# Kernel optimization log

Hardware: AMD Instinct MI355X
Metric: run time of the kernel (lower is better)

## Reference

```python
import jax, jax.numpy as jnp
import numpy as np

B, S, DM, H, DK, DV = 2, 2048, 1024, 16, 64, 64

def setup_inputs() -> dict:
    key = jax.random.key(0)
    ks = jax.random.split(key, 12)
    s = 0.02
    return {
        "Q": jax.random.normal(ks[0], (B, S, DM), jnp.float32),
        "K": jax.random.normal(ks[1], (B, S, DM), jnp.float32),
        "V": jax.random.normal(ks[2], (B, S, DM), jnp.float32),
        "mask": jax.random.randint(ks[3], (B, S, S), 0, 2).astype(bool),
        "wq": jax.random.normal(ks[4], (DM, H * DK), jnp.float32) * s,
        "bq": jnp.zeros((H * DK,), jnp.float32),
        "wk": jax.random.normal(ks[5], (DM, H * DK), jnp.float32) * s,
        "bk": jnp.zeros((H * DK,), jnp.float32),
        "wv": jax.random.normal(ks[6], (DM, H * DV), jnp.float32) * s,
        "bv": jnp.zeros((H * DV,), jnp.float32),
        "wo": jax.random.normal(ks[7], (H * DV, DM), jnp.float32) * s,
        "bo": jnp.zeros((DM,), jnp.float32),
    }

def reference(Q, K, V, mask, wq, bq, wk, bk, wv, bv, wo, bo):
    b = Q.shape[0]
    # projections -> [b, h, s, d]
    q = (Q @ wq + bq).reshape(b, -1, H, DK).transpose(0, 2, 1, 3)
    k = (K @ wk + bk).reshape(b, -1, H, DK).transpose(0, 2, 1, 3)
    v = (V @ wv + bv).reshape(b, -1, H, DV).transpose(0, 2, 1, 3)
    # scaled dot-product attention with boolean mask (True = masked out)
    scores = jnp.einsum("bhqd,bhkd->bhqk", q, k) / jnp.sqrt(jnp.float32(DK))
    scores = jnp.where(mask[:, None, :, :], jnp.float32(-1e9), scores)
    attn = jax.nn.softmax(scores, axis=-1)  # [b,h,s,s]
    ctx = jnp.einsum("bhqk,bhkd->bhqd", attn, v)
    ctx = ctx.transpose(0, 2, 1, 3).reshape(b, -1, H * DV)
    out = ctx @ wo + bo  # [b, s, d_model]
    return out, attn
```

## Files before the change

kernel.cpp:

```cpp
#include <hip/hip_runtime.h>

typedef unsigned short u16;
typedef unsigned int u32;
typedef unsigned long long u64;
typedef __attribute__((ext_vector_type(8))) short bf16x8;
typedef __attribute__((ext_vector_type(4))) float f32x4;

#define NB 2
#define NS 2048
#define NDM 1024
#define NH 16

#define MFMA_B16(a, b, c) __builtin_amdgcn_mfma_f32_16x16x32_bf16(a, b, c, 0, 0, 0)

__device__ __forceinline__ u16 f2bf(float f) {
  union { float f; unsigned u; } v; v.f = f;
  return (u16)((v.u + 0x7fffu + ((v.u >> 16) & 1u)) >> 16);
}

__global__ __launch_bounds__(256) void cast_bf16(const float* __restrict__ in,
                                                 u16* __restrict__ out, int n4) {
  int i = blockIdx.x * 256 + threadIdx.x;
  if (i < n4) {
    const float4 v = reinterpret_cast<const float4*>(in)[i];
    ushort4 o; o.x = f2bf(v.x); o.y = f2bf(v.y); o.z = f2bf(v.z); o.w = f2bf(v.w);
    reinterpret_cast<ushort4*>(out)[i] = o;
  }
}

__global__ __launch_bounds__(256) void transpose_w(const float* __restrict__ in,
                                                   u16* __restrict__ out) {
  __shared__ float tile[32][33];
  int bx = blockIdx.x, by = blockIdx.y;
  int x = threadIdx.x & 31, y0 = threadIdx.x >> 5;
#pragma unroll
  for (int i = 0; i < 4; i++) {
    int y = y0 + i * 8;
    tile[y][x] = in[(by * 32 + y) * NDM + bx * 32 + x];
  }
  __syncthreads();
#pragma unroll
  for (int i = 0; i < 4; i++) {
    int y = y0 + i * 8;
    out[(bx * 32 + y) * NDM + by * 32 + x] = f2bf(tile[x][y]);
  }
}

__global__ __launch_bounds__(256) void mask2bits(const u32* __restrict__ mask, u32* __restrict__ mb) {
  int idx = blockIdx.x * 256 + threadIdx.x;
  u32 mw0 = mask[threadIdx.x & 63];
  bool floatmode = (__ballot(mw0 == 0x3F800000u) != 0ull);
  bool bytemode = !floatmode && (__ballot((mw0 >> 8) != 0u) != 0ull);
  int row = idx >> 6;
  int wword = idx & 63;
  u32 bits = 0;
  if (!bytemode) {
    const uint4* p = reinterpret_cast<const uint4*>(mask + (size_t)row * 2048 + wword * 32);
#pragma unroll
    for (int i = 0; i < 8; i++) {
      uint4 v = p[i];
      bits |= (v.x ? 1u : 0u) << (i * 4 + 0);
      bits |= (v.y ? 1u : 0u) << (i * 4 + 1);
      bits |= (v.z ? 1u : 0u) << (i * 4 + 2);
      bits |= (v.w ? 1u : 0u) << (i * 4 + 3);
    }
  } else {
    const uint4* p = reinterpret_cast<const uint4*>(
        reinterpret_cast<const unsigned char*>(mask) + (size_t)row * 2048 + wword * 32);
#pragma unroll
    for (int i = 0; i < 2; i++) {
      uint4 v = p[i];
      u32 wsv[4] = {v.x, v.y, v.z, v.w};
#pragma unroll
      for (int j = 0; j < 4; j++)
#pragma unroll
        for (int kq = 0; kq < 4; kq++)
          bits |= ((((wsv[j] >> (kq * 8)) & 0xffu) != 0u) ? 1u : 0u) << (i * 16 + j * 4 + kq);
    }
  }
  mb[idx] = bits;
}

struct GArgs { const u16* X; const u16* W; const float* bias; void* out; int mode; float scale; };

__global__ __launch_bounds__(256, 2) void gemm_bt(GArgs g0, GArgs g1, GArgs g2) {
  GArgs ga = (blockIdx.z == 0) ? g0 : (blockIdx.z == 1 ? g1 : g2);
  const int K = 1024, N = 1024;
  __shared__ u16 As[128 * 32];
  __shared__ u16 Bs[128 * 32];
  const int t = threadIdx.x, w = t >> 6, l = t & 63;
  const int m0 = blockIdx.x * 128, n0 = blockIdx.y * 128;
  const int wm = (w >> 1) * 64, wn = (w & 1) * 64;
  const f32x4 fz = {0.f, 0.f, 0.f, 0.f};
  f32x4 acc[4][4];
#pragma unroll
  for (int i = 0; i < 4; i++)
#pragma unroll
    for (int j = 0; j < 4; j++) acc[i][j] = fz;

  for (int k0 = 0; k0 < K; k0 += 32) {
#pragma unroll
    for (int i = 0; i < 2; i++) {
      int idx = i * 256 + w * 64 + l;
      int r = idx >> 2, c = (idx & 3) * 8;
      __builtin_amdgcn_global_load_lds(
          reinterpret_cast<const unsigned*>(ga.X + (size_t)(m0 + r) * K + k0 + c),
          reinterpret_cast<unsigned*>(&As[(i * 256 + w * 64) * 8]), 16, 0, 0);
      __builtin_amdgcn_global_load_lds(
          reinterpret_cast<const unsigned*>(ga.W + (size_t)(n0 + r) * K + k0 + c),
          reinterpret_cast<unsigned*>(&Bs[(i * 256 + w * 64) * 8]), 16, 0, 0);
    }
    __syncthreads();
    bf16x8 af[4], bfr[4];
#pragma unroll
    for (int mt = 0; mt < 4; mt++)
      af[mt] = *reinterpret_cast<const bf16x8*>(&As[(wm + mt * 16 + (l & 15)) * 32 + (l >> 4) * 8]);
#pragma unroll
    for (int nt = 0; nt < 4; nt++)
      bfr[nt] = *reinterpret_cast<const bf16x8*>(&Bs[(wn + nt * 16 + (l & 15)) * 32 + (l >> 4) * 8]);
#pragma unroll
    for (int mt = 0; mt < 4; mt++)
#pragma unroll
      for (int nt = 0; nt < 4; nt++)
        acc[mt][nt] = MFMA_B16(af[mt], bfr[nt], acc[mt][nt]);
    __syncthreads();
  }

#pragma unroll
  for (int nt = 0; nt < 4; nt++) {
    int n = n0 + wn + nt * 16 + (l & 15);
    float bias = ga.bias[n];
#pragma unroll
    for (int mt = 0; mt < 4; mt++) {
      int mb = m0 + wm + mt * 16 + ((l >> 4) << 2);
#pragma unroll
      for (int r = 0; r < 4; r++) {
        int m = mb + r;
        float v = (acc[mt][nt][r] + bias) * ga.scale;
        if (ga.mode == 2) {
          reinterpret_cast<float*>(ga.out)[(size_t)m * N + n] = v;
        } else {
          int b = m >> 11, s = m & 2047, h = n >> 6, d = n & 63;
          if (ga.mode == 0)
            reinterpret_cast<u16*>(ga.out)[(((size_t)(b * NH + h) * NS + s) << 6) + d] = f2bf(v);
          else
            reinterpret_cast<u16*>(ga.out)[((size_t)(b * NH + h) * 64 + d) * NS + s] = f2bf(v);
        }
      }
    }
  }
}

__global__ __launch_bounds__(256, 4) void attn_kernel(
    const u16* __restrict__ qh, const u16* __restrict__ kh, const u16* __restrict__ vT,
    const u32* __restrict__ mb, float* __restrict__ attn, u16* __restrict__ ctx) {
  __shared__ u16 Ks[2][32 * 64];
  __shared__ u16 Vs[2][64 * 32];
  __shared__ u16 Ps[4][16 * 40];
  __shared__ float Pf[4][16 * 36];
  const int tid = threadIdx.x, w = tid >> 6, l = tid & 63;
  int id = blockIdx.x;
  int wgid = (id & 7) * 128 + (id >> 3);
  int qt = wgid & 31, pr = wgid >> 5;
  int h = pr & 15, b = pr >> 4;
  const size_t head = (size_t)b * NH + h;
  const u16* qp = qh + head * NS * 64;
  const u16* kp = kh + head * NS * 64;
  const u16* vp = vT + head * 64 * NS;
  const int qr0 = qt * 64 + w * 16;
  const int lo = l & 15, hi = l >> 4;
  const int rbase = hi << 2;
  const f32x4 fz = {0.f, 0.f, 0.f, 0.f};

  bf16x8 aq0, aq1;
  {
    const u16* p = qp + (size_t)(qr0 + lo) * 64 + hi * 8;
    aq0 = *reinterpret_cast<const bf16x8*>(p);
    aq1 = *reinterpret_cast<const bf16x8*>(p + 32);
  }
  const u32* mrow = mb + ((size_t)b * NS + qr0 + rbase) * 64;

  const int k_row = tid >> 3, k_slot = tid & 7;
  const u16* ksrc0 = kp + (size_t)k_row * 64 + ((k_slot ^ (k_row & 7)) * 8);
  const int v_dv = tid >> 2, v_slot = tid & 3;
  const u16* vsrc0 = vp + (size_t)v_dv * NS + ((v_slot ^ ((v_dv >> 1) & 3)) * 8);

  const int sxk = lo & 7;
  const int sxv = (lo >> 1) & 3;

  float rs0 = 0.f, rs1 = 0.f, rs2 = 0.f, rs3 = 0.f;

  __builtin_amdgcn_global_load_lds(reinterpret_cast<const unsigned*>(ksrc0),
                                   reinterpret_cast<unsigned*>(&Ks[0][w * 512]), 16, 0, 0);
  asm volatile("s_waitcnt vmcnt(0)" ::: "memory");
  __builtin_amdgcn_s_barrier();
  asm volatile("" ::: "memory");

  for (int t = 0; t < 64; ++t) {
    const u16* kbase = &Ks[t & 1][0];
    u16* kdst = &Ks[(t + 1) & 1][w * 512];
    __builtin_amdgcn_global_load_lds(
        reinterpret_cast<const unsigned*>(ksrc0 + (size_t)(t + 1) * 2048),
        reinterpret_cast<unsigned*>(kdst), 16, 0, 0);
    asm volatile("" ::: "memory");
    u32 m0 = mrow[t], m1 = mrow[64 + t], m2 = mrow[128 + t], m3 = mrow[192 + t];
    bf16x8 b00 = *reinterpret_cast<const bf16x8*>(&kbase[(lo) * 64 + ((hi ^ sxk) * 8)]);
    bf16x8 b01 = *reinterpret_cast<const bf16x8*>(&kbase[(lo) * 64 + (((4 + hi) ^ sxk) * 8)]);
    bf16x8 b10 = *reinterpret_cast<const bf16x8*>(&kbase[(16 + lo) * 64 + ((hi ^ sxk) * 8)]);
    bf16x8 b11 = *reinterpret_cast<const bf16x8*>(&kbase[(16 + lo) * 64 + (((4 + hi) ^ sxk) * 8)]);
    f32x4 s0 = MFMA_B16(aq1, b01, MFMA_B16(aq0, b00, fz));
    f32x4 s1 = MFMA_B16(aq1, b11, MFMA_B16(aq0, b10, fz));
    rs0 += ((m0 >> lo) & 1u) ? 0.f : __expf(s0[0]);
    rs1 += ((m1 >> lo) & 1u) ? 0.f : __expf(s0[1]);
    rs2 += ((m2 >> lo) & 1u) ? 0.f : __expf(s0[2]);
    rs3 += ((m3 >> lo) & 1u) ? 0.f : __expf(s0[3]);
    int bit1 = 16 + lo;
    rs0 += ((m0 >> bit1) & 1u) ? 0.f : __expf(s1[0]);
    rs1 += ((m1 >> bit1) & 1u) ? 0.f : __expf(s1[1]);
    rs2 += ((m2 >> bit1) & 1u) ? 0.f : __expf(s1[2]);
    rs3 += ((m3 >> bit1) & 1u) ? 0.f : __expf(s1[3]);
    asm volatile("s_waitcnt vmcnt(4)" ::: "memory");
    __builtin_amdgcn_s_barrier();
    asm volatile("" ::: "memory");
  }

  {
    float v;
    v = rs0; v += __shfl_xor(v, 1); v += __shfl_xor(v, 2); v += __shfl_xor(v, 4); v += __shfl_xor(v, 8);
    rs0 = 1.f / fmaxf(v, 1e-30f);
    v = rs1; v += __shfl_xor(v, 1); v += __shfl_xor(v, 2); v += __shfl_xor(v, 4); v += __shfl_xor(v, 8);
    rs1 = 1.f / fmaxf(v, 1e-30f);
    v = rs2; v += __shfl_xor(v, 1); v += __shfl_xor(v, 2); v += __shfl_xor(v, 4); v += __shfl_xor(v, 8);
    rs2 = 1.f / fmaxf(v, 1e-30f);
    v = rs3; v += __shfl_xor(v, 1); v += __shfl_xor(v, 2); v += __shfl_xor(v, 4); v += __shfl_xor(v, 8);
    rs3 = 1.f / fmaxf(v, 1e-30f);
  }

  f32x4 c0 = fz, c1 = fz, c2 = fz, c3 = fz;
  float* abase = attn + (head * NS + qr0) * NS;
  float* pfw = &Pf[w][0];
  u16* psw = &Ps[w][0];
  const int srow = l >> 2, schunk = l & 3;

  __builtin_amdgcn_global_load_lds(reinterpret_cast<const unsigned*>(ksrc0),
                                   reinterpret_cast<unsigned*>(&Ks[0][w * 512]), 16, 0, 0);
  __builtin_amdgcn_global_load_lds(reinterpret_cast<const unsigned*>(vsrc0),
                                   reinterpret_cast<unsigned*>(&Vs[0][w * 512]), 16, 0, 0);
  asm volatile("s_waitcnt vmcnt(0)" ::: "memory");
  __builtin_amdgcn_s_barrier();
  asm volatile("" ::: "memory");

  for (int t = 0; t < 64; ++t) {
    const u16* kbase = &Ks[t & 1][0];
    const u16* vbase = &Vs[t & 1][0];
    u16* kdst = &Ks[(t + 1) & 1][w * 512];
    u16* vdst = &Vs[(t + 1) & 1][w * 512];
    __builtin_amdgcn_global_load_lds(
        reinterpret_cast<const unsigned*>(ksrc0 + (size_t)(t + 1) * 2048),
        reinterpret_cast<unsigned*>(kdst), 16, 0, 0);
    __builtin_amdgcn_global_load_lds(
        reinterpret_cast<const unsigned*>(vsrc0 + (size_t)(t + 1) * 32),
        reinterpret_cast<unsigned*>(vdst), 16, 0, 0);
    asm volatile("" ::: "memory");
    u32 m0 = mrow[t], m1 = mrow[64 + t], m2 = mrow[128 + t], m3 = mrow[192 + t];
    bf16x8 b00 = *reinterpret_cast<const bf16x8*>(&kbase[(lo) * 64 + ((hi ^ sxk) * 8)]);
    bf16x8 b01 = *reinterpret_cast<const bf16x8*>(&kbase[(lo) * 64 + (((4 + hi) ^ sxk) * 8)]);
    bf16x8 b10 = *reinterpret_cast<const bf16x8*>(&kbase[(16 + lo) * 64 + ((hi ^ sxk) * 8)]);
    bf16x8 b11 = *reinterpret_cast<const bf16x8*>(&kbase[(16 + lo) * 64 + (((4 + hi) ^ sxk) * 8)]);
    f32x4 s0 = MFMA_B16(aq1, b01, MFMA_B16(aq0, b00, fz));
    f32x4 s1 = MFMA_B16(aq1, b11, MFMA_B16(aq0, b10, fz));
    float p;
    p = ((m0 >> lo) & 1u) ? 0.f : __expf(s0[0]) * rs0;
    pfw[(rbase + 0) * 36 + lo] = p; psw[(rbase + 0) * 40 + lo] = f2bf(p);
    p = ((m1 >> lo) & 1u) ? 0.f : __expf(s0[1]) * rs1;
    pfw[(rbase + 1) * 36 + lo] = p; psw[(rbase + 1) * 40 + lo] = f2bf(p);
    p = ((m2 >> lo) & 1u) ? 0.f : __expf(s0[2]) * rs2;
    pfw[(rbase + 2) * 36 + lo] = p; psw[(rbase + 2) * 40 + lo] = f2bf(p);
    p = ((m3 >> lo) & 1u) ? 0.f : __expf(s0[3]) * rs3;
    pfw[(rbase + 3) * 36 + lo] = p; psw[(rbase + 3) * 40 + lo] = f2bf(p);
    int bit1 = 16 + lo;
    p = ((m0 >> bit1) & 1u) ? 0.f : __expf(s1[0]) * rs0;
    pfw[(rbase + 0) * 36 + 16 + lo] = p; psw[(rbase + 0) * 40 + 16 + lo] = f2bf(p);
    p = ((m1 >> bit1) & 1u) ? 0.f : __expf(s1[1]) * rs1;
    pfw[(rbase + 1) * 36 + 16 + lo] = p; psw[(rbase + 1) * 40 + 16 + lo] = f2bf(p);
    p = ((m2 >> bit1) & 1u) ? 0.f : __expf(s1[2]) * rs2;
    pfw[(rbase + 2) * 36 + 16 + lo] = p; psw[(rbase + 2) * 40 + 16 + lo] = f2bf(p);
    p = ((m3 >> bit1) & 1u) ? 0.f : __expf(s1[3]) * rs3;
    pfw[(rbase + 3) * 36 + 16 + lo] = p; psw[(rbase + 3) * 40 + 16 + lo] = f2bf(p);
    bf16x8 pa = *reinterpret_cast<const bf16x8*>(&psw[lo * 40 + hi * 8]);
    bf16x8 v0 = *reinterpret_cast<const bf16x8*>(&vbase[(lo) * 32 + ((hi ^ sxv) * 8)]);
    bf16x8 v1 = *reinterpret_cast<const bf16x8*>(&vbase[(16 + lo) * 32 + ((hi ^ sxv) * 8)]);
    bf16x8 v2 = *reinterpret_cast<const bf16x8*>(&vbase[(32 + lo) * 32 + ((hi ^ sxv) * 8)]);
    bf16x8 v3 = *reinterpret_cast<const bf16x8*>(&vbase[(48 + lo) * 32 + ((hi ^ sxv) * 8)]);
    c0 = MFMA_B16(pa, v0, c0);
    c1 = MFMA_B16(pa, v1, c1);
    c2 = MFMA_B16(pa, v2, c2);
    c3 = MFMA_B16(pa, v3, c3);
    f32x4 o0 = *reinterpret_cast<const f32x4*>(&pfw[srow * 36 + schunk * 4]);
    f32x4 o1 = *reinterpret_cast<const f32x4*>(&pfw[srow * 36 + (schunk + 4) * 4]);
    *reinterpret_cast<f32x4*>(abase + (size_t)srow * NS + t * 32 + schunk * 4) = o0;
    *reinterpret_cast<f32x4*>(abase + (size_t)srow * NS + t * 32 + (schunk + 4) * 4) = o1;
    asm volatile("s_waitcnt vmcnt(6)" ::: "memory");
    __builtin_amdgcn_s_barrier();
    asm volatile("" ::: "memory");
  }

#define CTXW(cv, ct)                                                                   \
  {                                                                                    \
    ctx[((size_t)b * NS + qr0 + rbase + 0) * 1024 + h * 64 + (ct)*16 + lo] = f2bf(cv[0]); \
    ctx[((size_t)b * NS + qr0 + rbase + 1) * 1024 + h * 64 + (ct)*16 + lo] = f2bf(cv[1]); \
    ctx[((size_t)b * NS + qr0 + rbase + 2) * 1024 + h * 64 + (ct)*16 + lo] = f2bf(cv[2]); \
    ctx[((size_t)b * NS + qr0 + rbase + 3) * 1024 + h * 64 + (ct)*16 + lo] = f2bf(cv[3]); \
  }
  CTXW(c0, 0) CTXW(c1, 1) CTXW(c2, 2) CTXW(c3, 3)
#undef CTXW
}

extern "C" void kernel_launch(void* const* d_in, const int* in_sizes, int n_in,
                              void* d_out, int out_size, void* d_ws, size_t ws_size,
                              hipStream_t stream) {
  const float* Q = (const float*)d_in[0];
  const float* K = (const float*)d_in[1];
  const float* V = (const float*)d_in[2];
  const u32* mask = (const u32*)d_in[3];
  const float* wq = (const float*)d_in[4];
  const float* bq = (const float*)d_in[5];
  const float* wk = (const float*)d_in[6];
  const float* bk = (const float*)d_in[7];
  const float* wv = (const float*)d_in[8];
  const float* bv = (const float*)d_in[9];
  const float* wo = (const float*)d_in[10];
  const float* bo = (const float*)d_in[11];
  float* out = (float*)d_out;
  float* attn = out + (size_t)NB * NS * NDM;

  char* ws = (char*)d_ws;
  u16* Qb  = (u16*)(ws + 0);
  u16* Kb  = (u16*)(ws + 8388608);
  u16* Vb  = (u16*)(ws + 16777216);
  u16* wqT = (u16*)(ws + 25165824);
  u16* wkT = (u16*)(ws + 27262976);
  u16* wvT = (u16*)(ws + 29360128);
  u16* woT = (u16*)(ws + 31457280);
  u16* qhd = (u16*)(ws + 33554432);
  u16* khd = (u16*)(ws + 41943040);
  u16* vTd = (u16*)(ws + 50331648);
  u16* ctx = (u16*)(ws + 58720256);
  u32* mbits = (u32*)(ws + 0);

  cast_bf16<<<4096, 256, 0, stream>>>(Q, Qb, 1048576);
  cast_bf16<<<4096, 256, 0, stream>>>(K, Kb, 1048576);
  cast_bf16<<<4096, 256, 0, stream>>>(V, Vb, 1048576);
  transpose_w<<<dim3(32, 32), 256, 0, stream>>>(wq, wqT);
  transpose_w<<<dim3(32, 32), 256, 0, stream>>>(wk, wkT);
  transpose_w<<<dim3(32, 32), 256, 0, stream>>>(wv, wvT);
  transpose_w<<<dim3(32, 32), 256, 0, stream>>>(wo, woT);

  GArgs gq = {Qb, wqT, bq, (void*)qhd, 0, 0.125f};
  GArgs gk = {Kb, wkT, bk, (void*)khd, 0, 1.0f};
  GArgs gv = {Vb, wvT, bv, (void*)vTd, 1, 1.0f};
  gemm_bt<<<dim3(32, 8, 3), 256, 0, stream>>>(gq, gk, gv);

  mask2bits<<<1024, 256, 0, stream>>>(mask, mbits);

  attn_kernel<<<1024, 256, 0, stream>>>(qhd, khd, vTd, mbits, attn, ctx);

  GArgs go = {ctx, woT, bo, d_out, 2, 1.0f};
  gemm_bt<<<dim3(32, 8, 1), 256, 0, stream>>>(go, go, go);
}
```

Baseline: 339.1 us.

## Merge prep launches, prefetch mask words, emit attn from bf16 P buffer

The three fp32-to-bf16 casts now run as one launch, and the four weight transposes run as one launch indexed by blockIdx.z, which cuts launch overhead. In the attention kernel, mask words for the next tile are loaded one iteration ahead so their global-load latency overlaps the current compute. The fp32 Pf shared-memory staging buffer is removed, and the attn output is rebuilt from the bf16 P tile. This saves LDS stores and LDS capacity, but the stored attention probabilities carry only bf16 precision, which risks accuracy tolerance.

```diff
diff --git a/kernel.cpp b/kernel.cpp
--- a/kernel.cpp
+++ b/kernel.cpp
@@ -17,20 +17,30 @@
   union { float f; unsigned u; } v; v.f = f;
   return (u16)((v.u + 0x7fffu + ((v.u >> 16) & 1u)) >> 16);
 }
-
-__global__ __launch_bounds__(256) void cast_bf16(const float* __restrict__ in,
-                                                 u16* __restrict__ out, int n4) {
+__device__ __forceinline__ float bf2f(u16 h) {
+  union { float f; unsigned u; } v; v.u = ((u32)h) << 16; return v.f;
+}
+
+__global__ __launch_bounds__(256) void cast3_bf16(const float* __restrict__ a,
+                                                  const float* __restrict__ b,
+                                                  const float* __restrict__ c,
+                                                  u16* __restrict__ oa, u16* __restrict__ ob,
+                                                  u16* __restrict__ oc) {
   int i = blockIdx.x * 256 + threadIdx.x;
-  if (i < n4) {
-    const float4 v = reinterpret_cast<const float4*>(in)[i];
-    ushort4 o; o.x = f2bf(v.x); o.y = f2bf(v.y); o.z = f2bf(v.z); o.w = f2bf(v.w);
-    reinterpret_cast<ushort4*>(out)[i] = o;
-  }
-}
-
-__global__ __launch_bounds__(256) void transpose_w(const float* __restrict__ in,
-                                                   u16* __restrict__ out) {
+  const float* src; u16* dst; int j;
+  if (i < 1048576) { src = a; dst = oa; j = i; }
+  else if (i < 2097152) { src = b; dst = ob; j = i - 1048576; }
+  else { src = c; dst = oc; j = i - 2097152; }
+  const float4 v = reinterpret_cast<const float4*>(src)[j];
+  ushort4 o; o.x = f2bf(v.x); o.y = f2bf(v.y); o.z = f2bf(v.z); o.w = f2bf(v.w);
+  reinterpret_cast<ushort4*>(dst)[j] = o;
+}
+
+struct TW4 { const float* in[4]; u16* out[4]; };
+__global__ __launch_bounds__(256) void transpose_w4(TW4 tw) {
   __shared__ float tile[32][33];
+  const float* in = tw.in[blockIdx.z];
+  u16* out = tw.out[blockIdx.z];
   int bx = blockIdx.x, by = blockIdx.y;
   int x = threadIdx.x & 31, y0 = threadIdx.x >> 5;
 #pragma unroll
@@ -157,7 +167,6 @@
   __shared__ u16 Ks[2][32 * 64];
   __shared__ u16 Vs[2][64 * 32];
   __shared__ u16 Ps[4][16 * 40];
-  __shared__ float Pf[4][16 * 36];
   const int tid = threadIdx.x, w = tid >> 6, l = tid & 63;
   int id = blockIdx.x;
   int wgid = (id & 7) * 128 + (id >> 3);
@@ -184,41 +193,47 @@
   const u16* ksrc0 = kp + (size_t)k_row * 64 + ((k_slot ^ (k_row & 7)) * 8);
   const int v_dv = tid >> 2, v_slot = tid & 3;
   const u16* vsrc0 = vp + (size_t)v_dv * NS + ((v_slot ^ ((v_dv >> 1) & 3)) * 8);
-
   const int sxk = lo & 7;
   const int sxv = (lo >> 1) & 3;
 
+#define STAGE_KT(tt)                                                                    \
+  __builtin_amdgcn_global_load_lds(                                                     \
+      reinterpret_cast<const unsigned*>(ksrc0 + (size_t)(tt) * 2048),                   \
+      reinterpret_cast<unsigned*>(&Ks[(tt) & 1][w * 512]), 16, 0, 0);
+#define STAGE_VT(tt)                                                                    \
+  __builtin_amdgcn_global_load_lds(                                                     \
+      reinterpret_cast<const unsigned*>(vsrc0 + (size_t)(tt) * 32),                     \
+      reinterpret_cast<unsigned*>(&Vs[(tt) & 1][w * 512]), 16, 0, 0);
+
   float rs0 = 0.f, rs1 = 0.f, rs2 = 0.f, rs3 = 0.f;
 
-  __builtin_amdgcn_global_load_lds(reinterpret_cast<const unsigned*>(ksrc0),
-                                   reinterpret_cast<unsigned*>(&Ks[0][w * 512]), 16, 0, 0);
+  u32 mc0 = mrow[0], mc1 = mrow[64], mc2 = mrow[128], mc3 = mrow[192];
+  STAGE_KT(0);
   asm volatile("s_waitcnt vmcnt(0)" ::: "memory");
   __builtin_amdgcn_s_barrier();
   asm volatile("" ::: "memory");
 
   for (int t = 0; t < 64; ++t) {
+    STAGE_KT(t + 1);
+    u32 mn0 = mrow[t + 1], mn1 = mrow[65 + t], mn2 = mrow[129 + t], mn3 = mrow[193 + t];
+    asm volatile("" ::: "memory");
     const u16* kbase = &Ks[t & 1][0];
-    u16* kdst = &Ks[(t + 1) & 1][w * 512];
-    __builtin_amdgcn_global_load_lds(
-        reinterpret_cast<const unsigned*>(ksrc0 + (size_t)(t + 1) * 2048),
-        reinterpret_cast<unsigned*>(kdst), 16, 0, 0);
-    asm volatile("" ::: "memory");
-    u32 m0 = mrow[t], m1 = mrow[64 + t], m2 = mrow[128 + t], m3 = mrow[192 + t];
     bf16x8 b00 = *reinterpret_cast<const bf16x8*>(&kbase[(lo) * 64 + ((hi ^ sxk) * 8)]);
     bf16x8 b01 = *reinterpret_cast<const bf16x8*>(&kbase[(lo) * 64 + (((4 + hi) ^ sxk) * 8)]);
     bf16x8 b10 = *reinterpret_cast<const bf16x8*>(&kbase[(16 + lo) * 64 + ((hi ^ sxk) * 8)]);
     bf16x8 b11 = *reinterpret_cast<const bf16x8*>(&kbase[(16 + lo) * 64 + (((4 + hi) ^ sxk) * 8)]);
     f32x4 s0 = MFMA_B16(aq1, b01, MFMA_B16(aq0, b00, fz));
     f32x4 s1 = MFMA_B16(aq1, b11, MFMA_B16(aq0, b10, fz));
-    rs0 += ((m0 >> lo) & 1u) ? 0.f : __expf(s0[0]);
-    rs1 += ((m1 >> lo) & 1u) ? 0.f : __expf(s0[1]);
-    rs2 += ((m2 >> lo) & 1u) ? 0.f : __expf(s0[2]);
-    rs3 += ((m3 >> lo) & 1u) ? 0.f : __expf(s0[3]);
+    rs0 += ((mc0 >> lo) & 1u) ? 0.f : __expf(s0[0]);
+    rs1 += ((mc1 >> lo) & 1u) ? 0.f : __expf(s0[1]);
+    rs2 += ((mc2 >> lo) & 1u) ? 0.f : __expf(s0[2]);
+    rs3 += ((mc3 >> lo) & 1u) ? 0.f : __expf(s0[3]);
     int bit1 = 16 + lo;
-    rs0 += ((m0 >> bit1) & 1u) ? 0.f : __expf(s1[0]);
-    rs1 += ((m1 >> bit1) & 1u) ? 0.f : __expf(s1[1]);
-    rs2 += ((m2 >> bit1) & 1u) ? 0.f : __expf(s1[2]);
-    rs3 += ((m3 >> bit1) & 1u) ? 0.f : __expf(s1[3]);
+    rs0 += ((mc0 >> bit1) & 1u) ? 0.f : __expf(s1[0]);
+    rs1 += ((mc1 >> bit1) & 1u) ? 0.f : __expf(s1[1]);
+    rs2 += ((mc2 >> bit1) & 1u) ? 0.f : __expf(s1[2]);
+    rs3 += ((mc3 >> bit1) & 1u) ? 0.f : __expf(s1[3]);
+    mc0 = mn0; mc1 = mn1; mc2 = mn2; mc3 = mn3;
     asm volatile("s_waitcnt vmcnt(4)" ::: "memory");
     __builtin_amdgcn_s_barrier();
     asm volatile("" ::: "memory");
@@ -238,31 +253,23 @@
 
   f32x4 c0 = fz, c1 = fz, c2 = fz, c3 = fz;
   float* abase = attn + (head * NS + qr0) * NS;
-  float* pfw = &Pf[w][0];
   u16* psw = &Ps[w][0];
   const int srow = l >> 2, schunk = l & 3;
 
-  __builtin_amdgcn_global_load_lds(reinterpret_cast<const unsigned*>(ksrc0),
-                                   reinterpret_cast<unsigned*>(&Ks[0][w * 512]), 16, 0, 0);
-  __builtin_amdgcn_global_load_lds(reinterpret_cast<const unsigned*>(vsrc0),
-                                   reinterpret_cast<unsigned*>(&Vs[0][w * 512]), 16, 0, 0);
+  mc0 = mrow[0]; mc1 = mrow[64]; mc2 = mrow[128]; mc3 = mrow[192];
+  STAGE_KT(0);
+  STAGE_VT(0);
   asm volatile("s_waitcnt vmcnt(0)" ::: "memory");
   __builtin_amdgcn_s_barrier();
   asm volatile("" ::: "memory");
 
   for (int t = 0; t < 64; ++t) {
+    STAGE_KT(t + 1);
+    STAGE_VT(t + 1);
+    u32 mn0 = mrow[t + 1], mn1 = mrow[65 + t], mn2 = mrow[129 + t], mn3 = mrow[193 + t];
+    asm volatile("" ::: "memory");
     const u16* kbase = &Ks[t & 1][0];
     const u16* vbase = &Vs[t & 1][0];
-    u16* kdst = &Ks[(t + 1) & 1][w * 512];
-    u16* vdst = &Vs[(t + 1) & 1][w * 512];
-    __builtin_amdgcn_global_load_lds(
-        reinterpret_cast<const unsigned*>(ksrc0 + (size_t)(t + 1) * 2048),
-        reinterpret_cast<unsigned*>(kdst), 16, 0, 0);
-    __builtin_amdgcn_global_load_lds(
-        reinterpret_cast<const unsigned*>(vsrc0 + (size_t)(t + 1) * 32),
-        reinterpret_cast<unsigned*>(vdst), 16, 0, 0);
-    asm volatile("" ::: "memory");
-    u32 m0 = mrow[t], m1 = mrow[64 + t], m2 = mrow[128 + t], m3 = mrow[192 + t];
     bf16x8 b00 = *reinterpret_cast<const bf16x8*>(&kbase[(lo) * 64 + ((hi ^ sxk) * 8)]);
     bf16x8 b01 = *reinterpret_cast<const bf16x8*>(&kbase[(lo) * 64 + (((4 + hi) ^ sxk) * 8)]);
     bf16x8 b10 = *reinterpret_cast<const bf16x8*>(&kbase[(16 + lo) * 64 + ((hi ^ sxk) * 8)]);
@@ -270,43 +277,43 @@
     f32x4 s0 = MFMA_B16(aq1, b01, MFMA_B16(aq0, b00, fz));
     f32x4 s1 = MFMA_B16(aq1, b11, MFMA_B16(aq0, b10, fz));
     float p;
-    p = ((m0 >> lo) & 1u) ? 0.f : __expf(s0[0]) * rs0;
-    pfw[(rbase + 0) * 36 + lo] = p; psw[(rbase + 0) * 40 + lo] = f2bf(p);
-    p = ((m1 >> lo) & 1u) ? 0.f : __expf(s0[1]) * rs1;
-    pfw[(rbase + 1) * 36 + lo] = p; psw[(rbase + 1) * 40 + lo] = f2bf(p);
-    p = ((m2 >> lo) & 1u) ? 0.f : __expf(s0[2]) * rs2;
-    pfw[(rbase + 2) * 36 + lo] = p; psw[(rbase + 2) * 40 + lo] = f2bf(p);
-    p = ((m3 >> lo) & 1u) ? 0.f : __expf(s0[3]) * rs3;
-    pfw[(rbase + 3) * 36 + lo] = p; psw[(rbase + 3) * 40 + lo] = f2bf(p);
+    p = ((mc0 >> lo) & 1u) ? 0.f : __expf(s0[0]) * rs0; psw[(rbase + 0) * 40 + lo] = f2bf(p);
+    p = ((mc1 >> lo) & 1u) ? 0.f : __expf(s0[1]) * rs1; psw[(rbase + 1) * 40 + lo] = f2bf(p);
+    p = ((mc2 >> lo) & 1u) ? 0.f : __expf(s0[2]) * rs2; psw[(rbase + 2) * 40 + lo] = f2bf(p);
+    p = ((mc3 >> lo) & 1u) ? 0.f : __expf(s0[3]) * rs3; psw[(rbase + 3) * 40 + lo] = f2bf(p);
     int bit1 = 16 + lo;
-    p = ((m0 >> bit1) & 1u) ? 0.f : __expf(s1[0]) * rs0;
-    pfw[(rbase + 0) * 36 + 16 + lo] = p; psw[(rbase + 0) * 40 + 16 + lo] = f2bf(p);
-    p = ((m1 >> bit1) & 1u) ? 0.f : __expf(s1[1]) * rs1;
-    pfw[(rbase + 1) * 36 + 16 + lo] = p; psw[(rbase + 1) * 40 + 16 + lo] = f2bf(p);
-    p = ((m2 >> bit1) & 1u) ? 0.f : __expf(s1[2]) * rs2;
-    pfw[(rbase + 2) * 36 + 16 + lo] = p; psw[(rbase + 2) * 40 + 16 + lo] = f2bf(p);
-    p = ((m3 >> bit1) & 1u) ? 0.f : __expf(s1[3]) * rs3;
-    pfw[(rbase + 3) * 36 + 16 + lo] = p; psw[(rbase + 3) * 40 + 16 + lo] = f2bf(p);
-    bf16x8 pa = *reinterpret_cast<const bf16x8*>(&psw[lo * 40 + hi * 8]);
-    bf16x8 v0 = *reinterpret_cast<const bf16x8*>(&vbase[(lo) * 32 + ((hi ^ sxv) * 8)]);
-    bf16x8 v1 = *reinterpret_cast<const bf16x8*>(&vbase[(16 + lo) * 32 + ((hi ^ sxv) * 8)]);
-    bf16x8 v2 = *reinterpret_cast<const bf16x8*>(&vbase[(32 + lo) * 32 + ((hi ^ sxv) * 8)]);
-    bf16x8 v3 = *reinterpret_cast<const bf16x8*>(&vbase[(48 + lo) * 32 + ((hi ^ sxv) * 8)]);
-    c0 = MFMA_B16(pa, v0, c0);
-    c1 = MFMA_B16(pa, v1, c1);
-    c2 = MFMA_B16(pa, v2, c2);
-    c3 = MFMA_B16(pa, v3, c3);
-    f32x4 o0 = *reinterpret_cast<const f32x4*>(&pfw[srow * 36 + schunk * 4]);
-    f32x4 o1 = *reinterpret_cast<const f32x4*>(&pfw[srow * 36 + (schunk + 4) * 4]);
-    *reinterpret_cast<f32x4*>(abase + (size_t)srow * NS + t * 32 + schunk * 4) = o0;
-    *reinterpret_cast<f32x4*>(abase + (size_t)srow * NS + t * 32 + (schunk + 4) * 4) = o1;
+    p = ((mc0 >> bit1) & 1u) ? 0.f : __expf(s1[0]) * rs0; psw[(rbase + 0) * 40 + 16 + lo] = f2bf(p);
+    p = ((mc1 >> bit1) & 1u) ? 0.f : __expf(s1[1]) * rs1; psw[(rbase + 1) * 40 + 16 + lo] = f2bf(p);
+    p = ((mc2 >> bit1) & 1u) ? 0.f : __expf(s1[2]) * rs2; psw[(rbase + 2) * 40 + 16 + lo] = f2bf(p);
+    p = ((mc3 >> bit1) & 1u) ? 0.f : __expf(s1[3]) * rs3; psw[(rbase + 3) * 40 + 16 + lo] = f2bf(p);
+    mc0 = mn0; mc1 = mn1; mc2 = mn2; mc3 = mn3;
+    {
+      bf16x8 pa = *reinterpret_cast<const bf16x8*>(&psw[lo * 40 + hi * 8]);
+      bf16x8 v0 = *reinterpret_cast<const bf16x8*>(&vbase[(lo) * 32 + ((hi ^ sxv) * 8)]);
+      bf16x8 v1 = *reinterpret_cast<const bf16x8*>(&vbase[(16 + lo) * 32 + ((hi ^ sxv) * 8)]);
+      bf16x8 v2 = *reinterpret_cast<const bf16x8*>(&vbase[(32 + lo) * 32 + ((hi ^ sxv) * 8)]);
+      bf16x8 v3 = *reinterpret_cast<const bf16x8*>(&vbase[(48 + lo) * 32 + ((hi ^ sxv) * 8)]);
+      c0 = MFMA_B16(pa, v0, c0);
+      c1 = MFMA_B16(pa, v1, c1);
+      c2 = MFMA_B16(pa, v2, c2);
+      c3 = MFMA_B16(pa, v3, c3);
+    }
+    {
+      float* arow = abase + (size_t)srow * NS + t * 32 + schunk * 8;
+      bf16x8 q0 = *reinterpret_cast<const bf16x8*>(&psw[srow * 40 + schunk * 8]);
+      f32x4 o0, o1;
+#pragma unroll
+      for (int j = 0; j < 4; ++j) { o0[j] = bf2f((u16)q0[j]); o1[j] = bf2f((u16)q0[j + 4]); }
+      *reinterpret_cast<f32x4*>(arow + 0) = o0;
+      *reinterpret_cast<f32x4*>(arow + 4) = o1;
+    }
     asm volatile("s_waitcnt vmcnt(6)" ::: "memory");
     __builtin_amdgcn_s_barrier();
     asm volatile("" ::: "memory");
   }
 
-#define CTXW(cv, ct)                                                                   \
-  {                                                                                    \
+#define CTXW(cv, ct)                                                                      \
+  {                                                                                       \
     ctx[((size_t)b * NS + qr0 + rbase + 0) * 1024 + h * 64 + (ct)*16 + lo] = f2bf(cv[0]); \
     ctx[((size_t)b * NS + qr0 + rbase + 1) * 1024 + h * 64 + (ct)*16 + lo] = f2bf(cv[1]); \
     ctx[((size_t)b * NS + qr0 + rbase + 2) * 1024 + h * 64 + (ct)*16 + lo] = f2bf(cv[2]); \
@@ -314,6 +321,8 @@
   }
   CTXW(c0, 0) CTXW(c1, 1) CTXW(c2, 2) CTXW(c3, 3)
 #undef CTXW
+#undef STAGE_KT
+#undef STAGE_VT
 }
 
 extern "C" void kernel_launch(void* const* d_in, const int* in_sizes, int n_in,
@@ -348,13 +357,11 @@
   u16* ctx = (u16*)(ws + 58720256);
   u32* mbits = (u32*)(ws + 0);
 
-  cast_bf16<<<4096, 256, 0, stream>>>(Q, Qb, 1048576);
-  cast_bf16<<<4096, 256, 0, stream>>>(K, Kb, 1048576);
-  cast_bf16<<<4096, 256, 0, stream>>>(V, Vb, 1048576);
-  transpose_w<<<dim3(32, 32), 256, 0, stream>>>(wq, wqT);
-  transpose_w<<<dim3(32, 32), 256, 0, stream>>>(wk, wkT);
-  transpose_w<<<dim3(32, 32), 256, 0, stream>>>(wv, wvT);
-  transpose_w<<<dim3(32, 32), 256, 0, stream>>>(wo, woT);
+  cast3_bf16<<<12288, 256, 0, stream>>>(Q, K, V, Qb, Kb, Vb);
+  TW4 tw;
+  tw.in[0] = wq; tw.in[1] = wk; tw.in[2] = wv; tw.in[3] = wo;
+  tw.out[0] = wqT; tw.out[1] = wkT; tw.out[2] = wvT; tw.out[3] = woT;
+  transpose_w4<<<dim3(32, 32, 4), 256, 0, stream>>>(tw);
 
   GArgs gq = {Qb, wqT, bq, (void*)qhd, 0, 0.125f};
   GArgs gk = {Kb, wkT, bk, (void*)khd, 0, 1.0f};
```

Measured after the change: 334.9 us. No clear change (-1.2%).
